# Optimization experiments

Hardware: AMD Instinct MI355X
Metric: run time of the kernel (lower is better)

The kernel has to match this reference:

```python
import jax, jax.numpy as jnp
import numpy as np

EPS = 1e-6
SCALE_A = 0.9999

def a_powers(A, t):
    # A: [K, n, n]; returns stack [I, A, ..., A^(t-1)] of shape [t, K, n, n] via repeated squaring.
    K, n, _ = A.shape
    eye = jnp.broadcast_to(jnp.eye(n, dtype=A.dtype), (K, n, n))
    result = jnp.stack([eye, A])
    lift = A @ A
    for _ in range(int(np.ceil(np.log2(t))) - 1):
        result = jnp.concatenate([result, result @ lift])
        lift = lift @ lift
    return result[:t]

def fast_conv_real(a, b):
    # a: [len1, K, n, n], b: [batch, len2, K, n] -> conv(b, a): [batch, len1+len2-1, K, n]
    len1 = a.shape[0]
    len2 = b.shape[1]
    T = 2 ** int(np.ceil(np.log2(len1 + len2 - 1)))
    Af = jnp.fft.rfft(a, n=T, axis=0)
    Bf = jnp.fft.rfft(b, n=T, axis=1)
    Cf = jnp.einsum('blki,lkij->blkj', Bf, Af)
    c = jnp.fft.irfft(Cf, n=T, axis=1)
    return c[:, :len1 + len2 - 1]

def rmsnorm(x, w):
    return x * jax.lax.rsqrt(jnp.mean(x * x, axis=-1, keepdims=True) + EPS) * w

def setup_inputs() -> dict:
    key = jax.random.key(0)
    ku, kx, kt, kb, kc = jax.random.split(key, 5)
    batch, length, input_size, state_size, output_size = 8, 4096, 1024, 512, 1024
    K = state_size // 2
    u = jax.random.normal(ku, (batch, length, input_size), dtype=jnp.float32)
    x0 = jax.random.normal(kx, (batch, K, 2), dtype=jnp.float32)
    theta = jax.random.uniform(kt, (K,), dtype=jnp.float32) * (2 * np.pi)
    c, s = jnp.cos(theta), jnp.sin(theta)
    # 2x2 rotation blocks: [[cos, sin], [-sin, cos]], scaled for stability
    A = SCALE_A * jnp.stack([jnp.stack([c, s], -1), jnp.stack([-s, c], -1)], -2)  # [K,2,2]
    B = jax.random.normal(kb, (input_size, state_size), dtype=jnp.float32) / (state_size + input_size) ** 0.5
    C = jax.random.normal(kc, (state_size, output_size), dtype=jnp.float32) / state_size ** 0.5
    norm_weight = jnp.ones((input_size,), dtype=jnp.float32)
    return {"u": u, "x0": x0, "A": A, "B": B, "C": C, "norm_weight": norm_weight}

def reference(u, x0, A, B, C, norm_weight):
    batch, length, _ = u.shape
    K = A.shape[0]
    un = rmsnorm(u, norm_weight)                           # [b, L, in]
    Aps = a_powers(A, length + 1)                          # [L+1, K, 2, 2]
    uB = (un @ B).reshape(batch, length, K, 2)             # [b, L, K, 2]
    x = fast_conv_real(Aps[:-1], uB)[:, :length]           # [b, L, K, 2]
    x = x + jnp.einsum('bki,lkij->blkj', x0, Aps[1:])      # initial-state response
    new_state = x[:, -1]                                   # [b, K, 2]
    y = x.reshape(batch, length, K * 2) @ C                # [b, L, out]
    return y, new_state
```

## Files before the change

### kernel.cpp

```cpp
#include <hip/hip_runtime.h>
#include <hip/hip_bf16.h>

typedef __attribute__((ext_vector_type(8))) short bf16x8;
typedef __attribute__((ext_vector_type(4))) float f32x4;
typedef __attribute__((ext_vector_type(4))) int int4v;

#define BATCH 8
#define LEN 4096
#define DIN 1024
#define DST 512
#define KHALF 256
#define DOUT 1024
#define NCHUNK 64
#define CHUNK 64

static __device__ __forceinline__ ushort f2bf(float f) {
    uint x = __float_as_uint(f);
    uint r = (x + 0x7fffu + ((x >> 16) & 1u)) >> 16;
    return (ushort)r;
}
static __device__ __forceinline__ float bf2f(ushort u) {
    return __uint_as_float((uint)u << 16);
}

#define GL16(gp, lp) __builtin_amdgcn_global_load_lds( \
    (const __attribute__((address_space(1))) void*)(gp), \
    (__attribute__((address_space(3))) void*)(lp), 16, 0, 0)

__global__ __launch_bounds__(256)
void rmsnorm_kernel(const float* __restrict__ u, const float* __restrict__ w,
                    ushort* __restrict__ un)
{
    const int row = blockIdx.x;
    const int t = threadIdx.x;
    const float4 v = ((const float4*)(u + (size_t)row * DIN))[t];
    float ss = v.x*v.x + v.y*v.y + v.z*v.z + v.w*v.w;
    #pragma unroll
    for (int m = 32; m >= 1; m >>= 1) ss += __shfl_xor(ss, m, 64);
    __shared__ float partial[4];
    if ((t & 63) == 0) partial[t >> 6] = ss;
    __syncthreads();
    const float total = partial[0] + partial[1] + partial[2] + partial[3];
    const float scale = rsqrtf(total * (1.0f / DIN) + 1e-6f);
    const float4 wv = ((const float4*)w)[t];
    ushort4 o;
    o.x = f2bf(v.x * scale * wv.x);
    o.y = f2bf(v.y * scale * wv.y);
    o.z = f2bf(v.z * scale * wv.z);
    o.w = f2bf(v.w * scale * wv.w);
    ((ushort4*)(un + (size_t)row * DIN))[t] = o;
}

__global__ __launch_bounds__(256)
void transpose_bf16_kernel(const float* __restrict__ src, ushort* __restrict__ dst,
                           int R, int C)
{
    const int id = blockIdx.x * 256 + threadIdx.x;
    if (id >= R * C) return;
    const int r = id / C, c = id % C;
    dst[(size_t)c * R + r] = f2bf(src[id]);
}

#define BM 128
#define BN 128
#define BK 64
__global__ __launch_bounds__(256, 3)
void gemm_bt_kernel(const ushort* __restrict__ A, const ushort* __restrict__ Bt,
                    void* __restrict__ Cout, int M, int N, int K, int Nt, int obf)
{
    __shared__ ushort sA[BM * BK];
    __shared__ ushort sB[BN * BK];
    const int tid = threadIdx.x;
    const int lane = tid & 63;
    const int wave = tid >> 6;
    const int wr = wave >> 1, wc = wave & 1;

    const int b = blockIdx.x;
    const int slot = b >> 3;
    const int mt = (b & 7) + 8 * (slot / Nt);
    const int nt = slot - (slot / Nt) * Nt;
    const int m0 = mt * BM, n0 = nt * BN;

    const size_t K2 = (size_t)K * 2;
    const int srow = tid >> 3;
    const int scol = ((tid & 7) << 4) ^ ((srow & 7) << 4);
    const char* gA = (const char*)A + (size_t)(m0 + srow) * K2 + scol;
    const char* gB = (const char*)Bt + (size_t)(n0 + srow) * K2 + scol;
    const int ldsBase = wave * 1024;

    f32x4 acc[4][4] = {};

    const int nkt = K / BK;
    for (int kt = 0; kt < nkt; ++kt) {
        __syncthreads();
        const size_t kOff = (size_t)kt * (BK * 2);
        #pragma unroll
        for (int c2 = 0; c2 < 4; ++c2) {
            GL16(gA + (size_t)c2 * 32 * K2 + kOff, (char*)sA + ldsBase + c2 * 4096);
            GL16(gB + (size_t)c2 * 32 * K2 + kOff, (char*)sB + ldsBase + c2 * 4096);
        }
        __syncthreads();
        #pragma unroll
        for (int kk = 0; kk < 2; ++kk) {
            bf16x8 af[4], bfr[4];
            #pragma unroll
            for (int i = 0; i < 4; ++i) {
                const int arow = wr * 64 + i * 16 + (lane & 15);
                const int aoff = arow * 128 + ((kk * 64 + (lane >> 4) * 16) ^ ((arow & 7) << 4));
                af[i] = *(const bf16x8*)((const char*)sA + aoff);
                const int brow = wc * 64 + i * 16 + (lane & 15);
                const int boff = brow * 128 + ((kk * 64 + (lane >> 4) * 16) ^ ((brow & 7) << 4));
                bfr[i] = *(const bf16x8*)((const char*)sB + boff);
            }
            #pragma unroll
            for (int i = 0; i < 4; ++i)
                #pragma unroll
                for (int j = 0; j < 4; ++j)
                    acc[i][j] = __builtin_amdgcn_mfma_f32_16x16x32_bf16(af[i], bfr[j], acc[i][j], 0, 0, 0);
        }
    }
    if (obf) {
        ushort* base = (ushort*)Cout;
        #pragma unroll
        for (int i = 0; i < 4; ++i) {
            #pragma unroll
            for (int j = 0; j < 4; ++j) {
                const int row = m0 + wr * 64 + i * 16 + (lane >> 4) * 4;
                const int col = n0 + wc * 64 + j * 16 + (lane & 15);
                ushort* cp = base + (size_t)row * N + col;
                #pragma unroll
                for (int r = 0; r < 4; ++r)
                    cp[(size_t)r * N] = f2bf(acc[i][j][r]);
            }
        }
    } else {
        float* base = (float*)Cout;
        #pragma unroll
        for (int i = 0; i < 4; ++i) {
            #pragma unroll
            for (int j = 0; j < 4; ++j) {
                const int row = m0 + wr * 64 + i * 16 + (lane >> 4) * 4;
                const int col = n0 + wc * 64 + j * 16 + (lane & 15);
                float* cp = base + (size_t)row * N + col;
                #pragma unroll
                for (int r = 0; r < 4; ++r)
                    cp[(size_t)r * N] = acc[i][j][r];
            }
        }
    }
}

__global__ __launch_bounds__(256)
void scan_local_kernel(const ushort* __restrict__ uB, const float* __restrict__ A,
                       float* __restrict__ L)
{
    const int c = blockIdx.x, b = blockIdx.y, k = threadIdx.x;
    const float a00 = A[4*k+0], a01 = A[4*k+1], a10 = A[4*k+2], a11 = A[4*k+3];
    const ushort2* p = (const ushort2*)uB + ((size_t)b * LEN + c * CHUNK) * KHALF + k;
    float s0 = 0.f, s1 = 0.f;
    #pragma unroll 8
    for (int j = 0; j < CHUNK; ++j) {
        const ushort2 uv = p[(size_t)j * KHALF];
        const float ux = bf2f(uv.x), uy = bf2f(uv.y);
        const float t0 = fmaf(s0, a00, fmaf(s1, a10, ux));
        const float t1 = fmaf(s0, a01, fmaf(s1, a11, uy));
        s0 = t0; s1 = t1;
    }
    ((float2*)L)[((size_t)b * NCHUNK + c) * KHALF + k] = make_float2(s0, s1);
}

__global__ __launch_bounds__(256)
void scan_carry_kernel(const float* __restrict__ L, const float* __restrict__ A,
                       const float* __restrict__ x0, float* __restrict__ carry)
{
    const int b = blockIdx.x, k = threadIdx.x;
    float m00 = A[4*k+0], m01 = A[4*k+1], m10 = A[4*k+2], m11 = A[4*k+3];
    #pragma unroll
    for (int i = 0; i < 6; ++i) {
        const float n00 = m00*m00 + m01*m10;
        const float n01 = m00*m01 + m01*m11;
        const float n10 = m10*m00 + m11*m10;
        const float n11 = m10*m01 + m11*m11;
        m00 = n00; m01 = n01; m10 = n10; m11 = n11;
    }
    float c0 = x0[((size_t)b * KHALF + k) * 2 + 0];
    float c1 = x0[((size_t)b * KHALF + k) * 2 + 1];
    for (int c = 0; c < NCHUNK; ++c) {
        ((float2*)carry)[((size_t)b * NCHUNK + c) * KHALF + k] = make_float2(c0, c1);
        const float2 Lc = ((const float2*)L)[((size_t)b * NCHUNK + c) * KHALF + k];
        const float t0 = c0 * m00 + c1 * m10 + Lc.x;
        const float t1 = c0 * m01 + c1 * m11 + Lc.y;
        c0 = t0; c1 = t1;
    }
}

__global__ __launch_bounds__(256)
void scan_final_kernel(const ushort* __restrict__ uB, const float* __restrict__ A,
                       const float* __restrict__ carry, ushort* __restrict__ xbf,
                       float* __restrict__ state_out)
{
    const int c = blockIdx.x, b = blockIdx.y, k = threadIdx.x;
    const float a00 = A[4*k+0], a01 = A[4*k+1], a10 = A[4*k+2], a11 = A[4*k+3];
    const float2 s = ((const float2*)carry)[((size_t)b * NCHUNK + c) * KHALF + k];
    float s0 = s.x, s1 = s.y;
    const ushort2* p = (const ushort2*)uB + ((size_t)b * LEN + c * CHUNK) * KHALF + k;
    uint* xp = (uint*)xbf + ((size_t)b * LEN + c * CHUNK) * KHALF + k;
    #pragma unroll 8
    for (int j = 0; j < CHUNK; ++j) {
        const ushort2 uv = p[(size_t)j * KHALF];
        const float ux = bf2f(uv.x), uy = bf2f(uv.y);
        const float t0 = fmaf(s0, a00, fmaf(s1, a10, ux));
        const float t1 = fmaf(s0, a01, fmaf(s1, a11, uy));
        s0 = t0; s1 = t1;
        xp[(size_t)j * KHALF] = (uint)f2bf(s0) | ((uint)f2bf(s1) << 16);
    }
    if (c == NCHUNK - 1) {
        ((float2*)state_out)[(size_t)b * KHALF + k] = make_float2(s0, s1);
    }
}

extern "C" void kernel_launch(void* const* d_in, const int* in_sizes, int n_in,
                              void* d_out, int out_size, void* d_ws, size_t ws_size,
                              hipStream_t stream)
{
    (void)in_sizes; (void)n_in; (void)out_size; (void)ws_size;
    const float* u  = (const float*)d_in[0];
    const float* x0 = (const float*)d_in[1];
    const float* A  = (const float*)d_in[2];
    const float* B  = (const float*)d_in[3];
    const float* C  = (const float*)d_in[4];
    const float* w  = (const float*)d_in[5];
    float* y_out = (float*)d_out;
    float* state_out = y_out + (size_t)BATCH * LEN * DOUT;

    char* ws = (char*)d_ws;
    ushort* un    = (ushort*)(ws + 0);
    ushort* Bt    = (ushort*)(ws + 67108864);
    ushort* Ct    = (ushort*)(ws + 68157440);
    ushort* uBbf  = (ushort*)(ws + 69206016);
    ushort* xbf   = (ushort*)(ws + 136314880);
    float*  L     = (float*)(ws + 169869312);
    float*  carry = (float*)(ws + 170917888);

    transpose_bf16_kernel<<<dim3((DIN * DST + 255) / 256), 256, 0, stream>>>(B, Bt, DIN, DST);
    transpose_bf16_kernel<<<dim3((DST * DOUT + 255) / 256), 256, 0, stream>>>(C, Ct, DST, DOUT);
    rmsnorm_kernel<<<dim3(BATCH * LEN), 256, 0, stream>>>(u, w, un);
    gemm_bt_kernel<<<dim3(256 * 4), 256, 0, stream>>>(un, Bt, (void*)uBbf, BATCH * LEN, DST, DIN, 4, 1);
    scan_local_kernel<<<dim3(NCHUNK, BATCH), 256, 0, stream>>>(uBbf, A, L);
    scan_carry_kernel<<<dim3(BATCH), 256, 0, stream>>>(L, A, x0, carry);
    scan_final_kernel<<<dim3(NCHUNK, BATCH), 256, 0, stream>>>(uBbf, A, carry, xbf, state_out);
    gemm_bt_kernel<<<dim3(256 * 8), 256, 0, stream>>>(xbf, Ct, (void*)y_out, BATCH * LEN, DOUT, DST, 8, 0);
}
```

Baseline: 340.6 us.

## Double-buffer GEMM LDS tiles and fold carry scan into final scan

The GEMM now keeps two LDS buffers for A and B. It prefetches the next K-tile while the current one feeds the MFMAs, which removes one barrier per iteration and overlaps global loads with compute. The separate 8-block serial carry kernel is removed: each final-scan block now recomputes its own incoming carry by walking the preceding chunk summaries. This trades a launch and a low-parallelism serial pass for redundant per-block work. Doubling LDS per block to 64KB may lower the number of resident blocks per CU compared with the launch-bounds target of 3.

```diff
diff --git a/kernel.cpp b/kernel.cpp
--- a/kernel.cpp
+++ b/kernel.cpp
@@ -3,7 +3,6 @@
 
 typedef __attribute__((ext_vector_type(8))) short bf16x8;
 typedef __attribute__((ext_vector_type(4))) float f32x4;
-typedef __attribute__((ext_vector_type(4))) int int4v;
 
 #define BATCH 8
 #define LEN 4096
@@ -68,8 +67,8 @@
 void gemm_bt_kernel(const ushort* __restrict__ A, const ushort* __restrict__ Bt,
                     void* __restrict__ Cout, int M, int N, int K, int Nt, int obf)
 {
-    __shared__ ushort sA[BM * BK];
-    __shared__ ushort sB[BN * BK];
+    __shared__ ushort sA[2][BM * BK];
+    __shared__ ushort sB[2][BN * BK];
     const int tid = threadIdx.x;
     const int lane = tid & 63;
     const int wave = tid >> 6;
@@ -91,15 +90,25 @@
     f32x4 acc[4][4] = {};
 
     const int nkt = K / BK;
+    {
+        const size_t kOff = 0;
+        #pragma unroll
+        for (int c2 = 0; c2 < 4; ++c2) {
+            GL16(gA + (size_t)c2 * 32 * K2 + kOff, (char*)sA[0] + ldsBase + c2 * 4096);
+            GL16(gB + (size_t)c2 * 32 * K2 + kOff, (char*)sB[0] + ldsBase + c2 * 4096);
+        }
+    }
     for (int kt = 0; kt < nkt; ++kt) {
+        const int cur = kt & 1;
         __syncthreads();
-        const size_t kOff = (size_t)kt * (BK * 2);
-        #pragma unroll
-        for (int c2 = 0; c2 < 4; ++c2) {
-            GL16(gA + (size_t)c2 * 32 * K2 + kOff, (char*)sA + ldsBase + c2 * 4096);
-            GL16(gB + (size_t)c2 * 32 * K2 + kOff, (char*)sB + ldsBase + c2 * 4096);
-        }
-        __syncthreads();
+        if (kt + 1 < nkt) {
+            const size_t kOff = (size_t)(kt + 1) * (BK * 2);
+            #pragma unroll
+            for (int c2 = 0; c2 < 4; ++c2) {
+                GL16(gA + (size_t)c2 * 32 * K2 + kOff, (char*)sA[cur ^ 1] + ldsBase + c2 * 4096);
+                GL16(gB + (size_t)c2 * 32 * K2 + kOff, (char*)sB[cur ^ 1] + ldsBase + c2 * 4096);
+            }
+        }
         #pragma unroll
         for (int kk = 0; kk < 2; ++kk) {
             bf16x8 af[4], bfr[4];
@@ -107,10 +116,10 @@
             for (int i = 0; i < 4; ++i) {
                 const int arow = wr * 64 + i * 16 + (lane & 15);
                 const int aoff = arow * 128 + ((kk * 64 + (lane >> 4) * 16) ^ ((arow & 7) << 4));
-                af[i] = *(const bf16x8*)((const char*)sA + aoff);
+                af[i] = *(const bf16x8*)((const char*)sA[cur] + aoff);
                 const int brow = wc * 64 + i * 16 + (lane & 15);
                 const int boff = brow * 128 + ((kk * 64 + (lane >> 4) * 16) ^ ((brow & 7) << 4));
-                bfr[i] = *(const bf16x8*)((const char*)sB + boff);
+                bfr[i] = *(const bf16x8*)((const char*)sB[cur] + boff);
             }
             #pragma unroll
             for (int i = 0; i < 4; ++i)
@@ -170,11 +179,13 @@
 }
 
 __global__ __launch_bounds__(256)
-void scan_carry_kernel(const float* __restrict__ L, const float* __restrict__ A,
-                       const float* __restrict__ x0, float* __restrict__ carry)
-{
-    const int b = blockIdx.x, k = threadIdx.x;
-    float m00 = A[4*k+0], m01 = A[4*k+1], m10 = A[4*k+2], m11 = A[4*k+3];
+void scan_final_kernel(const ushort* __restrict__ uB, const float* __restrict__ A,
+                       const float* __restrict__ L, const float* __restrict__ x0,
+                       ushort* __restrict__ xbf, float* __restrict__ state_out)
+{
+    const int c = blockIdx.x, b = blockIdx.y, k = threadIdx.x;
+    const float a00 = A[4*k+0], a01 = A[4*k+1], a10 = A[4*k+2], a11 = A[4*k+3];
+    float m00 = a00, m01 = a01, m10 = a10, m11 = a11;
     #pragma unroll
     for (int i = 0; i < 6; ++i) {
         const float n00 = m00*m00 + m01*m10;
@@ -183,26 +194,14 @@
         const float n11 = m10*m01 + m11*m11;
         m00 = n00; m01 = n01; m10 = n10; m11 = n11;
     }
-    float c0 = x0[((size_t)b * KHALF + k) * 2 + 0];
-    float c1 = x0[((size_t)b * KHALF + k) * 2 + 1];
-    for (int c = 0; c < NCHUNK; ++c) {
-        ((float2*)carry)[((size_t)b * NCHUNK + c) * KHALF + k] = make_float2(c0, c1);
-        const float2 Lc = ((const float2*)L)[((size_t)b * NCHUNK + c) * KHALF + k];
-        const float t0 = c0 * m00 + c1 * m10 + Lc.x;
-        const float t1 = c0 * m01 + c1 * m11 + Lc.y;
-        c0 = t0; c1 = t1;
-    }
-}
-
-__global__ __launch_bounds__(256)
-void scan_final_kernel(const ushort* __restrict__ uB, const float* __restrict__ A,
-                       const float* __restrict__ carry, ushort* __restrict__ xbf,
-                       float* __restrict__ state_out)
-{
-    const int c = blockIdx.x, b = blockIdx.y, k = threadIdx.x;
-    const float a00 = A[4*k+0], a01 = A[4*k+1], a10 = A[4*k+2], a11 = A[4*k+3];
-    const float2 s = ((const float2*)carry)[((size_t)b * NCHUNK + c) * KHALF + k];
-    float s0 = s.x, s1 = s.y;
+    float s0 = x0[((size_t)b * KHALF + k) * 2 + 0];
+    float s1 = x0[((size_t)b * KHALF + k) * 2 + 1];
+    for (int j = 0; j < c; ++j) {
+        const float2 Lj = ((const float2*)L)[((size_t)b * NCHUNK + j) * KHALF + k];
+        const float t0 = s0 * m00 + s1 * m10 + Lj.x;
+        const float t1 = s0 * m01 + s1 * m11 + Lj.y;
+        s0 = t0; s1 = t1;
+    }
     const ushort2* p = (const ushort2*)uB + ((size_t)b * LEN + c * CHUNK) * KHALF + k;
     uint* xp = (uint*)xbf + ((size_t)b * LEN + c * CHUNK) * KHALF + k;
     #pragma unroll 8
@@ -240,14 +239,12 @@
     ushort* uBbf  = (ushort*)(ws + 69206016);
     ushort* xbf   = (ushort*)(ws + 136314880);
     float*  L     = (float*)(ws + 169869312);
-    float*  carry = (float*)(ws + 170917888);
 
     transpose_bf16_kernel<<<dim3((DIN * DST + 255) / 256), 256, 0, stream>>>(B, Bt, DIN, DST);
     transpose_bf16_kernel<<<dim3((DST * DOUT + 255) / 256), 256, 0, stream>>>(C, Ct, DST, DOUT);
     rmsnorm_kernel<<<dim3(BATCH * LEN), 256, 0, stream>>>(u, w, un);
     gemm_bt_kernel<<<dim3(256 * 4), 256, 0, stream>>>(un, Bt, (void*)uBbf, BATCH * LEN, DST, DIN, 4, 1);
     scan_local_kernel<<<dim3(NCHUNK, BATCH), 256, 0, stream>>>(uBbf, A, L);
-    scan_carry_kernel<<<dim3(BATCH), 256, 0, stream>>>(L, A, x0, carry);
-    scan_final_kernel<<<dim3(NCHUNK, BATCH), 256, 0, stream>>>(uBbf, A, carry, xbf, state_out);
+    scan_final_kernel<<<dim3(NCHUNK, BATCH), 256, 0, stream>>>(uBbf, A, L, x0, xbf, state_out);
     gemm_bt_kernel<<<dim3(256 * 8), 256, 0, stream>>>(xbf, Ct, (void*)y_out, BATCH * LEN, DOUT, DST, 8, 0);
 }
```

Result: slower. 349.9 us (+2.7%).
